# Performance work log

Measured on AMD Instinct MI355X. Metric: run time of the kernel, lower is better.

The kernel has to match this reference:

```python
import jax, jax.numpy as jnp
import numpy as np

H = 4          # number of GCN heads (hard-coded self.h = 4)
EPS = 1e-6     # MWPToolkit LayerNorm eps
B, K, D, HID = 16, 1024, 256, 256
DK = D // H


def setup_inputs() -> dict:
    key = jax.random.key(0)
    ks = jax.random.split(key, 12)
    sc = lambda fan_in: 1.0 / np.sqrt(fan_in).astype(np.float32)
    return {
        "graph_nodes": jax.random.normal(ks[0], (B, K, D), jnp.float32),
        "graph": jax.random.randint(ks[1], (B, 5, K, K), 0, 2, jnp.int32),
        # per-head GCN layer 1: GraphConvolution(indim -> hiddim)
        "Wg1": jax.random.normal(ks[2], (H, D, HID), jnp.float32) * sc(D),
        "bg1": jax.random.normal(ks[3], (H, HID), jnp.float32) * sc(D),
        # per-head GCN layer 2: GraphConvolution(hiddim -> d_k)
        "Wg2": jax.random.normal(ks[4], (H, HID, DK), jnp.float32) * sc(HID),
        "bg2": jax.random.normal(ks[5], (H, DK), jnp.float32) * sc(HID),
        # PositionwiseFeedForward: Linear(indim,hiddim) -> ReLU -> Linear(hiddim,outdim)
        "Wf1": jax.random.normal(ks[6], (D, HID), jnp.float32) * sc(D),
        "bf1": jax.random.normal(ks[7], (HID,), jnp.float32) * sc(D),
        "Wf2": jax.random.normal(ks[8], (HID, D), jnp.float32) * sc(HID),
        "bf2": jax.random.normal(ks[9], (D,), jnp.float32) * sc(HID),
        # LayerNorm(outdim) affine params
        "ln_a": jnp.ones((D,), jnp.float32),
        "ln_b": jnp.zeros((D,), jnp.float32),
    }


def reference(graph_nodes, graph, Wg1, bg1, Wg2, bg2, Wf1, bf1, Wf2, bf2, ln_a, ln_b):
    adj = graph.astype(jnp.float32)                      # (B, 5, K, K)
    # adj_list = [adj[:,1], adj[:,1], adj[:,4], adj[:,4]] -> stack heads
    adj_h = jnp.stack([adj[:, 1], adj[:, 1], adj[:, 4], adj[:, 4]])  # (H,B,K,K)

    # GCN layer 1 (all heads at once): relu(adj @ (x @ W1) + b1)
    sup1 = jnp.einsum('bkd,hdf->hbkf', graph_nodes, Wg1)            # (H,B,K,HID)
    h1 = jax.nn.relu(jnp.einsum('hbkj,hbjf->hbkf', adj_h, sup1)
                     + bg1[:, None, None, :])
    # (dropout is identity in eval)
    # GCN layer 2: adj @ (h1 @ W2) + b2
    sup2 = jnp.einsum('hbkf,hfe->hbke', h1, Wg2)                    # (H,B,K,DK)
    h2 = jnp.einsum('hbkj,hbje->hbke', adj_h, sup2) + bg2[:, None, None, :]

    # concat heads along feature dim: (B,K,H*DK) == (B,K,D)
    g = jnp.transpose(h2, (1, 2, 0, 3)).reshape(h2.shape[1], h2.shape[2], -1)

    # MWPToolkit LayerNorm: a*(x-mean)/(std+eps)+b, std unbiased (ddof=1)
    mu = g.mean(-1, keepdims=True)
    sd = jnp.std(g, axis=-1, keepdims=True, ddof=1)
    g = ln_a * (g - mu) / (sd + EPS) + ln_b + graph_nodes           # residual

    # PositionwiseFeedForward + residual (dropout identity in eval)
    ff = jax.nn.relu(g @ Wf1 + bf1) @ Wf2 + bf2
    out = ff + g
    return adj, out
```

## Files before the change

kernel.cpp:

```cpp
#include <hip/hip_runtime.h>

typedef unsigned short ushort_t;
using short8  = __attribute__((ext_vector_type(8))) short;
using floatx4 = __attribute__((ext_vector_type(4))) float;

__device__ __forceinline__ ushort_t f2bf(float f) {
  unsigned int x = __builtin_bit_cast(unsigned int, f);
  x += 0x7fffu + ((x >> 16) & 1u);
  return (ushort_t)(x >> 16);
}

__device__ __forceinline__ void gld16(const ushort_t* g, ushort_t* l) {
  __builtin_amdgcn_global_load_lds(
      (const __attribute__((address_space(1))) void*)(unsigned long long)(uintptr_t)g,
      (__attribute__((address_space(3))) void*)l, 16, 0, 0);
}

__global__ __launch_bounds__(256) void k_prep(const int* __restrict__ graph,
                                              float* __restrict__ adj_out,
                                              ushort_t* __restrict__ adjb,
                                              const float* __restrict__ gn,
                                              ushort_t* __restrict__ XT,
                                              const float* __restrict__ Wg1, const float* __restrict__ Wg2,
                                              const float* __restrict__ Wf1, const float* __restrict__ Wf2,
                                              ushort_t* __restrict__ W1T, ushort_t* __restrict__ W2pT,
                                              ushort_t* __restrict__ Wf1T, ushort_t* __restrict__ Wf2T) {
  __shared__ float t[64][68];
  const int bid = blockIdx.x;
  if (bid < 81920) {
    const size_t i = (size_t)bid * 256 + threadIdx.x;
    int4 v = ((const int4*)graph)[i];
    float4 f = make_float4((float)v.x, (float)v.y, (float)v.z, (float)v.w);
    ((float4*)adj_out)[i] = f;
    const size_t e0 = i * 4;
    const unsigned sb = (unsigned)(e0 >> 20);
    const unsigned s = sb % 5u, b = sb / 5u;
    if (s == 1u || s == 4u) {
      const unsigned tt = (s == 4u) ? 1u : 0u;
      ushort4 h;
      h.x = f2bf(f.x); h.y = f2bf(f.y); h.z = f2bf(f.z); h.w = f2bf(f.w);
      *(ushort4*)(adjb + (((size_t)(b * 2 + tt)) << 20) + (e0 & 0xFFFFFu)) = h;
    }
  } else if (bid < 82944) {
    const int id = bid - 81920;
    const int kt = id & 15, dt = (id >> 4) & 3, b = id >> 6;
    const int r  = threadIdx.x >> 4;
    const int c4 = (threadIdx.x & 15) * 4;
#pragma unroll
    for (int rr = 0; rr < 4; rr++) {
      const int kl = rr * 16 + r;
      float4 v = *(const float4*)(gn + ((size_t)(b * 1024 + kt * 64 + kl)) * 256 + dt * 64 + c4);
      t[kl][c4] = v.x; t[kl][c4 + 1] = v.y; t[kl][c4 + 2] = v.z; t[kl][c4 + 3] = v.w;
    }
    __syncthreads();
#pragma unroll
    for (int rr = 0; rr < 4; rr++) {
      const int dl = rr * 16 + r;
      ushort4 h;
      h.x = f2bf(t[c4][dl]);     h.y = f2bf(t[c4 + 1][dl]);
      h.z = f2bf(t[c4 + 2][dl]); h.w = f2bf(t[c4 + 3][dl]);
      *(ushort4*)(XT + ((size_t)(b * 256 + dt * 64 + dl)) * 1024 + kt * 64 + c4) = h;
    }
  } else {
    const int i = (bid - 82944) * 256 + threadIdx.x;
    if (i < 262144) {
      const int fI = i >> 8, d = i & 255;
      const int h = fI >> 8, ff = fI & 255;
      W1T[i] = f2bf(Wg1[((h << 8) + d) * 256 + ff]);
    } else if (i < 393216) {
      const int j = i - 262144;
      const int tt = j >> 16, rem = j & 65535;
      const int ep = rem >> 9, k = rem & 511;
      const int hh = ep >> 6;
      const float v = ((k >> 8) == hh)
          ? Wg2[(((tt * 2 + hh) << 8) + (k & 255)) * 64 + (ep & 63)] : 0.f;
      W2pT[j] = f2bf(v);
    } else if (i < 458752) {
      const int j = i - 393216;
      const int n = j >> 8, k = j & 255;
      Wf1T[j] = f2bf(Wf1[k * 256 + n]);
    } else if (i < 524288) {
      const int j = i - 458752;
      const int n = j >> 8, k = j & 255;
      Wf2T[j] = f2bf(Wf2[k * 256 + n]);
    }
  }
}

__global__ __launch_bounds__(256) void k_mid(const ushort_t* __restrict__ adjb,
                                             const ushort_t* __restrict__ XT,
                                             const ushort_t* __restrict__ W1T,
                                             const float* __restrict__ bg1,
                                             const ushort_t* __restrict__ W2pT,
                                             ushort_t* __restrict__ sup2T) {
  __shared__ ushort_t As[64 * 64];
  __shared__ ushort_t Bs[256 * 64];
  __shared__ ushort_t AXs[64 * 256];
  ushort_t* Hs = Bs + 8192;

  const int mt = blockIdx.x, bt = blockIdx.y;
  const int b = bt >> 1, t = bt & 1;
  const int tid = threadIdx.x, wave = tid >> 6, lane = tid & 63;
  const int l15 = lane & 15, quad = lane >> 4;
  const int wm = wave >> 1, wn = wave & 1;
  const int srow8 = lane >> 3, schunk = lane & 7;
  const int gcol = (schunk ^ srow8) * 8;
  const int cx = l15 & 7;

  const ushort_t* gA = adjb + ((size_t)bt << 20) + (size_t)(mt * 64 + wave * 16 + srow8) * 1024 + gcol;
  const ushort_t* gB = XT + ((size_t)b << 18) + (size_t)(wave * 64 + srow8) * 1024 + gcol;
  ushort_t* lA = As + (wave * 16) * 64;
  ushort_t* lB = Bs + (wave * 64) * 64;

  floatx4 acc1[2][8] = {};
  const int arow1 = (wm * 32 + l15) * 64;
  const int brow1 = (wn * 128 + l15) * 64;

  for (int k0 = 0; k0 < 1024; k0 += 64) {
#pragma unroll
    for (int ci = 0; ci < 2; ci++) gld16(gA + (size_t)(ci * 8) * 1024, lA + ci * 512);
#pragma unroll
    for (int ci = 0; ci < 8; ci++) gld16(gB + (size_t)(ci * 8) * 1024, lB + ci * 512);
    gA += 64; gB += 64;
    __syncthreads();
#pragma unroll
    for (int ks = 0; ks < 2; ks++) {
      const int cs = ((ks * 4 + quad) ^ cx) * 8;
      short8 af[2], bfr[8];
#pragma unroll
      for (int i = 0; i < 2; i++) af[i]  = *(const short8*)(As + arow1 + i * 1024 + cs);
#pragma unroll
      for (int j = 0; j < 8; j++) bfr[j] = *(const short8*)(Bs + brow1 + j * 1024 + cs);
#pragma unroll
      for (int i = 0; i < 2; i++)
#pragma unroll
        for (int j = 0; j < 8; j++)
          acc1[i][j] = __builtin_amdgcn_mfma_f32_16x16x32_bf16(af[i], bfr[j], acc1[i][j], 0, 0, 0);
    }
    __syncthreads();
  }

#pragma unroll
  for (int i = 0; i < 2; i++)
#pragma unroll
    for (int j = 0; j < 8; j++)
#pragma unroll
      for (int r = 0; r < 4; r++) {
        const int row = wm * 32 + i * 16 + quad * 4 + r;
        const int d   = wn * 128 + j * 16 + l15;
        AXs[row * 256 + ((((d >> 3) ^ row) & 31) << 3) + (d & 7)] = f2bf(acc1[i][j][r]);
      }
  __syncthreads();

  floatx4 acc4[4][2] = {};

#pragma unroll 1
  for (int nn = 0; nn < 4; nn++) {
    const int fg = t * 512 + nn * 128;

    floatx4 acc3[2][4] = {};
    for (int k0 = 0; k0 < 256; k0 += 64) {
#pragma unroll
      for (int ci = 0; ci < 4; ci++)
        gld16(W1T + (size_t)(fg + wave * 32 + ci * 8 + srow8) * 256 + k0 + gcol,
              Bs + (wave * 32 + ci * 8) * 64);
      __syncthreads();
#pragma unroll
      for (int ks = 0; ks < 2; ks++) {
        const int c32 = (k0 >> 3) + ks * 4 + quad;
        const int cs = ((ks * 4 + quad) ^ cx) * 8;
        short8 af[2], bfr[4];
#pragma unroll
        for (int i = 0; i < 2; i++) {
          const int row = wm * 32 + i * 16 + l15;
          af[i] = *(const short8*)(AXs + row * 256 + (((c32 ^ row) & 31) << 3));
        }
#pragma unroll
        for (int j = 0; j < 4; j++)
          bfr[j] = *(const short8*)(Bs + (wn * 64 + j * 16 + l15) * 64 + cs);
#pragma unroll
        for (int i = 0; i < 2; i++)
#pragma unroll
          for (int j = 0; j < 4; j++)
            acc3[i][j] = __builtin_amdgcn_mfma_f32_16x16x32_bf16(af[i], bfr[j], acc3[i][j], 0, 0, 0);
      }
      __syncthreads();
    }

#pragma unroll
    for (int j = 0; j < 4; j++) {
      const int fl = wn * 64 + j * 16 + l15;
      const float bj = bg1[fg + fl];
#pragma unroll
      for (int i = 0; i < 2; i++)
#pragma unroll
        for (int r = 0; r < 4; r++) {
          const int row = wm * 32 + i * 16 + quad * 4 + r;
          const float v = fmaxf(acc3[i][j][r] + bj, 0.f);
          Hs[row * 128 + ((((fl >> 3) ^ row) & 15) << 3) + (fl & 7)] = f2bf(v);
        }
    }
    __syncthreads();

    for (int k0 = 0; k0 < 128; k0 += 64) {
#pragma unroll
      for (int ci = 0; ci < 4; ci++)
        gld16(W2pT + (size_t)t * 65536 + (size_t)(wave * 32 + ci * 8 + srow8) * 512 + nn * 128 + k0 + gcol,
              Bs + (wave * 32 + ci * 8) * 64);
      __syncthreads();
#pragma unroll
      for (int ks = 0; ks < 2; ks++) {
        const int c32h = (k0 >> 3) + ks * 4 + quad;
        const int cs = ((ks * 4 + quad) ^ cx) * 8;
        short8 af[4], bfr[2];
#pragma unroll
        for (int i = 0; i < 4; i++)
          af[i] = *(const short8*)(Bs + (wm * 64 + i * 16 + l15) * 64 + cs);
#pragma unroll
        for (int j = 0; j < 2; j++) {
          const int row = wn * 32 + j * 16 + l15;
          bfr[j] = *(const short8*)(Hs + row * 128 + (((c32h ^ row) & 15) << 3));
        }
#pragma unroll
        for (int i = 0; i < 4; i++)
#pragma unroll
          for (int j = 0; j < 2; j++)
            acc4[i][j] = __builtin_amdgcn_mfma_f32_16x16x32_bf16(af[i], bfr[j], acc4[i][j], 0, 0, 0);
      }
      __syncthreads();
    }
  }

#pragma unroll
  for (int i = 0; i < 4; i++)
#pragma unroll
    for (int j = 0; j < 2; j++)
#pragma unroll
      for (int r = 0; r < 4; r++) {
        const int ep = wm * 64 + i * 16 + quad * 4 + r;
        const int kp = mt * 64 + wn * 32 + j * 16 + l15;
        sup2T[(size_t)bt * 131072 + (size_t)ep * 1024 + kp] = f2bf(acc4[i][j][r]);
      }
}

__global__ __launch_bounds__(256) void k_tail(const ushort_t* __restrict__ adjb,
                                              const ushort_t* __restrict__ sup2T,
                                              const float* __restrict__ bg2,
                                              const float* __restrict__ gn,
                                              const float* __restrict__ la,
                                              const float* __restrict__ lb,
                                              const ushort_t* __restrict__ Wf1T,
                                              const float* __restrict__ bf1,
                                              const ushort_t* __restrict__ Wf2T,
                                              const float* __restrict__ bf2,
                                              float* __restrict__ out) {
  __shared__ ushort_t As[64 * 64];
  __shared__ ushort_t Bs[256 * 64];
  __shared__ ushort_t Ps[32 * 256];
  __shared__ ushort_t Ts[32 * 256];
  __shared__ float sred[4][32], qred[4][32];

  const int mt = blockIdx.x, b = blockIdx.y;
  const int tid = threadIdx.x, wave = tid >> 6, lane = tid & 63;
  const int l15 = lane & 15, quad = lane >> 4;
  const int wn = wave;
  const int tsel = wn >> 1;

  const int srow8 = lane >> 3, schunk = lane & 7;
  const int gcol = (schunk ^ srow8) * 8;

  const ushort_t* gA = adjb + ((size_t)(b * 2 + (wave >> 1)) << 20)
                     + (size_t)(mt * 32 + (wave & 1) * 16 + srow8) * 1024 + gcol;
  const ushort_t* gB = sup2T + (size_t)(b * 2 + (wave >> 1)) * 131072
                     + (size_t)((wave & 1) * 64 + srow8) * 1024 + gcol;
  ushort_t* lA = As + (wave * 16) * 64;
  ushort_t* lB = Bs + (wave * 64) * 64;

  floatx4 acc[2][4] = {};
  const int arow0 = (tsel * 32 + l15) * 64;
  const int brow0 = (wn * 64 + l15) * 64;
  const int cx = l15 & 7;

  for (int k0 = 0; k0 < 1024; k0 += 64) {
#pragma unroll
    for (int ci = 0; ci < 2; ci++)
      gld16(gA + (size_t)(ci * 8) * 1024, lA + ci * 512);
#pragma unroll
    for (int ci = 0; ci < 8; ci++)
      gld16(gB + (size_t)(ci * 8) * 1024, lB + ci * 512);
    gA += 64; gB += 64;
    __syncthreads();
#pragma unroll
    for (int ks = 0; ks < 2; ks++) {
      const int cs = ((ks * 4 + quad) ^ cx) * 8;
      short8 af[2], bfr[4];
#pragma unroll
      for (int i = 0; i < 2; i++) af[i]  = *(const short8*)(As + arow0 + i * 1024 + cs);
#pragma unroll
      for (int j = 0; j < 4; j++) bfr[j] = *(const short8*)(Bs + brow0 + j * 1024 + cs);
#pragma unroll
      for (int i = 0; i < 2; i++)
#pragma unroll
        for (int j = 0; j < 4; j++)
          acc[i][j] = __builtin_amdgcn_mfma_f32_16x16x32_bf16(af[i], bfr[j], acc[i][j], 0, 0, 0);
    }
    __syncthreads();
  }

  float laj[4], lbj[4];
#pragma unroll
  for (int j = 0; j < 4; j++) {
    const int colg = wn * 64 + j * 16 + l15;
    const float bj = bg2[colg];
    laj[j] = la[colg]; lbj[j] = lb[colg];
#pragma unroll
    for (int i = 0; i < 2; i++)
#pragma unroll
      for (int r = 0; r < 4; r++) acc[i][j][r] += bj;
  }
#pragma unroll
  for (int i = 0; i < 2; i++)
#pragma unroll
    for (int r = 0; r < 4; r++) {
      float s = 0.f, q = 0.f;
#pragma unroll
      for (int j = 0; j < 4; j++) { const float v = acc[i][j][r]; s += v; q += v * v; }
#pragma unroll
      for (int m = 1; m < 16; m <<= 1) { s += __shfl_xor(s, m); q += __shfl_xor(q, m); }
      if (l15 == 0) {
        const int row = i * 16 + quad * 4 + r;
        sred[wn][row] = s; qred[wn][row] = q;
      }
    }
  __syncthreads();

  const size_t rowbase = (size_t)(b * 1024 + mt * 32);
  float glnreg[2][4][4];
#pragma unroll
  for (int i = 0; i < 2; i++)
#pragma unroll
    for (int r = 0; r < 4; r++) {
      const int row = i * 16 + quad * 4 + r;
      const float S = sred[0][row] + sred[1][row] + sred[2][row] + sred[3][row];
      const float Q = qred[0][row] + qred[1][row] + qred[2][row] + qred[3][row];
      const float mu = S * (1.f / 256.f);
      const float var = fmaxf((Q - S * mu) * (1.f / 255.f), 0.f);
      const float inv = 1.f / (sqrtf(var) + 1e-6f);
      const float* gnr = gn + (rowbase + row) * 256;
#pragma unroll
      for (int j = 0; j < 4; j++) {
        const int colg = wn * 64 + j * 16 + l15;
        const float g = laj[j] * (acc[i][j][r] - mu) * inv + lbj[j] + gnr[colg];
        glnreg[i][j][r] = g;
        Ps[row * 256 + ((((colg >> 3) ^ row) & 31) << 3) + (colg & 7)] = f2bf(g);
      }
    }
  __syncthreads();

  floatx4 acc2[2][4] = {};
  for (int k0 = 0; k0 < 256; k0 += 64) {
#pragma unroll
    for (int ci = 0; ci < 8; ci++)
      gld16(Wf1T + (size_t)(wave * 64 + ci * 8 + srow8) * 256 + k0 + gcol,
            Bs + (wave * 64 + ci * 8) * 64);
    __syncthreads();
#pragma unroll
    for (int ks = 0; ks < 2; ks++) {
      const int c32 = (k0 >> 3) + ks * 4 + quad;
      const int cs = ((ks * 4 + quad) ^ cx) * 8;
      short8 af[2], bfr[4];
#pragma unroll
      for (int i = 0; i < 2; i++) {
        const int row = i * 16 + l15;
        af[i] = *(const short8*)(Ps + row * 256 + (((c32 ^ row) & 31) << 3));
      }
#pragma unroll
      for (int j = 0; j < 4; j++) bfr[j] = *(const short8*)(Bs + brow0 + j * 1024 + cs);
#pragma unroll
      for (int i = 0; i < 2; i++)
#pragma unroll
        for (int j = 0; j < 4; j++)
          acc2[i][j] = __builtin_amdgcn_mfma_f32_16x16x32_bf16(af[i], bfr[j], acc2[i][j], 0, 0, 0);
    }
    __syncthreads();
  }

#pragma unroll
  for (int j = 0; j < 4; j++) {
    const int colg = wn * 64 + j * 16 + l15;
    const float bj = bf1[colg];
#pragma unroll
    for (int i = 0; i < 2; i++)
#pragma unroll
      for (int r = 0; r < 4; r++) {
        const int row = i * 16 + quad * 4 + r;
        const float v = fmaxf(acc2[i][j][r] + bj, 0.f);
        Ts[row * 256 + ((((colg >> 3) ^ row) & 31) << 3) + (colg & 7)] = f2bf(v);
      }
  }
  __syncthreads();

  floatx4 acc3[2][4] = {};
  for (int k0 = 0; k0 < 256; k0 += 64) {
#pragma unroll
    for (int ci = 0; ci < 8; ci++)
      gld16(Wf2T + (size_t)(wave * 64 + ci * 8 + srow8) * 256 + k0 + gcol,
            Bs + (wave * 64 + ci * 8) * 64);
    __syncthreads();
#pragma unroll
    for (int ks = 0; ks < 2; ks++) {
      const int c32 = (k0 >> 3) + ks * 4 + quad;
      const int cs = ((ks * 4 + quad) ^ cx) * 8;
      short8 af[2], bfr[4];
#pragma unroll
      for (int i = 0; i < 2; i++) {
        const int row = i * 16 + l15;
        af[i] = *(const short8*)(Ts + row * 256 + (((c32 ^ row) & 31) << 3));
      }
#pragma unroll
      for (int j = 0; j < 4; j++) bfr[j] = *(const short8*)(Bs + brow0 + j * 1024 + cs);
#pragma unroll
      for (int i = 0; i < 2; i++)
#pragma unroll
        for (int j = 0; j < 4; j++)
          acc3[i][j] = __builtin_amdgcn_mfma_f32_16x16x32_bf16(af[i], bfr[j], acc3[i][j], 0, 0, 0);
    }
    __syncthreads();
  }

#pragma unroll
  for (int j = 0; j < 4; j++) {
    const int colg = wn * 64 + j * 16 + l15;
    const float bj = bf2[colg];
#pragma unroll
    for (int i = 0; i < 2; i++)
#pragma unroll
      for (int r = 0; r < 4; r++) {
        const int row = i * 16 + quad * 4 + r;
        out[(rowbase + row) * 256 + colg] = acc3[i][j][r] + bj + glnreg[i][j][r];
      }
  }
}

extern "C" void kernel_launch(void* const* d_in, const int* in_sizes, int n_in,
                              void* d_out, int out_size, void* d_ws, size_t ws_size,
                              hipStream_t stream) {
  const float* gnodes = (const float*)d_in[0];
  const int*   graph  = (const int*)d_in[1];
  const float* Wg1 = (const float*)d_in[2];
  const float* bg1 = (const float*)d_in[3];
  const float* Wg2 = (const float*)d_in[4];
  const float* bg2 = (const float*)d_in[5];
  const float* Wf1 = (const float*)d_in[6];
  const float* bf1 = (const float*)d_in[7];
  const float* Wf2 = (const float*)d_in[8];
  const float* bf2 = (const float*)d_in[9];
  const float* ln_a = (const float*)d_in[10];
  const float* ln_b = (const float*)d_in[11];

  float* adj_out = (float*)d_out;
  float* out     = (float*)d_out + 83886080;

  char* ws = (char*)d_ws;
  ushort_t* adjb  = (ushort_t*)(ws);
  ushort_t* XT    = (ushort_t*)(ws + 67108864);
  ushort_t* W1T   = (ushort_t*)(ws + 75497472);
  ushort_t* W2pT  = (ushort_t*)(ws + 76021760);
  ushort_t* Wf1T  = (ushort_t*)(ws + 76283904);
  ushort_t* Wf2T  = (ushort_t*)(ws + 76414976);
  ushort_t* sup2T = (ushort_t*)(ws + 76546048);

  k_prep<<<84992, 256, 0, stream>>>(graph, adj_out, adjb, gnodes, XT,
                                    Wg1, Wg2, Wf1, Wf2, W1T, W2pT, Wf1T, Wf2T);

  k_mid<<<dim3(16, 32), 256, 0, stream>>>(adjb, XT, W1T, bg1, W2pT, sup2T);

  k_tail<<<dim3(32, 16), 256, 0, stream>>>(adjb, sup2T, bg2, gnodes, ln_a, ln_b,
                                           Wf1T, bf1, Wf2T, bf2, out);
}
```

Measured before the change: 656.5 us.

## Double-buffer GEMM main loops and prefetch weight tiles in GCN kernels

Rewrites the adjacency-GEMM K loops in k_mid and k_tail as two-stage ping-pong pipelines. The next tile's global-to-LDS loads are issued before the current tile's MFMAs, with a single waitcnt+barrier per stage replacing the paired __syncthreads. Weight tiles for the follow-on GEMMs (W1, W2, Wf1, Wf2) are also prefetched ahead of the epilogues. It further adds launch_bounds min-2-blocks occupancy hints and nontemporal loads/stores for the large adjacency conversion and the output. The aim is to hide global memory latency behind MFMA work. The cost is more LDS aliasing, and the FFN loops refill a shared weight buffer without a block barrier, which risks cross-wave races.

```diff
diff --git a/kernel.cpp b/kernel.cpp
--- a/kernel.cpp
+++ b/kernel.cpp
@@ -3,6 +3,8 @@
 typedef unsigned short ushort_t;
 using short8  = __attribute__((ext_vector_type(8))) short;
 using floatx4 = __attribute__((ext_vector_type(4))) float;
+using intx4   = __attribute__((ext_vector_type(4))) int;
+using fx4     = __attribute__((ext_vector_type(4))) float;
 
 __device__ __forceinline__ ushort_t f2bf(float f) {
   unsigned int x = __builtin_bit_cast(unsigned int, f);
@@ -14,6 +16,20 @@
   __builtin_amdgcn_global_load_lds(
       (const __attribute__((address_space(1))) void*)(unsigned long long)(uintptr_t)g,
       (__attribute__((address_space(3))) void*)l, 16, 0, 0);
+}
+
+__device__ __forceinline__ void wait_bar() {
+  asm volatile("s_waitcnt vmcnt(0)" ::: "memory");
+  __builtin_amdgcn_s_barrier();
+  __builtin_amdgcn_sched_barrier(0);
+}
+__device__ __forceinline__ void vwait0() {
+  asm volatile("s_waitcnt vmcnt(0)" ::: "memory");
+  __builtin_amdgcn_sched_barrier(0);
+}
+__device__ __forceinline__ void lwait0() {
+  asm volatile("s_waitcnt lgkmcnt(0)" ::: "memory");
+  __builtin_amdgcn_sched_barrier(0);
 }
 
 __global__ __launch_bounds__(256) void k_prep(const int* __restrict__ graph,
@@ -29,16 +45,16 @@
   const int bid = blockIdx.x;
   if (bid < 81920) {
     const size_t i = (size_t)bid * 256 + threadIdx.x;
-    int4 v = ((const int4*)graph)[i];
-    float4 f = make_float4((float)v.x, (float)v.y, (float)v.z, (float)v.w);
-    ((float4*)adj_out)[i] = f;
+    intx4 v = __builtin_nontemporal_load((const intx4*)graph + i);
+    fx4 f; f[0] = (float)v[0]; f[1] = (float)v[1]; f[2] = (float)v[2]; f[3] = (float)v[3];
+    __builtin_nontemporal_store(f, (fx4*)adj_out + i);
     const size_t e0 = i * 4;
     const unsigned sb = (unsigned)(e0 >> 20);
     const unsigned s = sb % 5u, b = sb / 5u;
     if (s == 1u || s == 4u) {
       const unsigned tt = (s == 4u) ? 1u : 0u;
       ushort4 h;
-      h.x = f2bf(f.x); h.y = f2bf(f.y); h.z = f2bf(f.z); h.w = f2bf(f.w);
+      h.x = f2bf(f[0]); h.y = f2bf(f[1]); h.z = f2bf(f[2]); h.w = f2bf(f[3]);
       *(ushort4*)(adjb + (((size_t)(b * 2 + tt)) << 20) + (e0 & 0xFFFFFu)) = h;
     }
   } else if (bid < 82944) {
@@ -87,16 +103,17 @@
   }
 }
 
-__global__ __launch_bounds__(256) void k_mid(const ushort_t* __restrict__ adjb,
-                                             const ushort_t* __restrict__ XT,
-                                             const ushort_t* __restrict__ W1T,
-                                             const float* __restrict__ bg1,
-                                             const ushort_t* __restrict__ W2pT,
-                                             ushort_t* __restrict__ sup2T) {
-  __shared__ ushort_t As[64 * 64];
-  __shared__ ushort_t Bs[256 * 64];
-  __shared__ ushort_t AXs[64 * 256];
+__global__ __launch_bounds__(256, 2) void k_mid(const ushort_t* __restrict__ adjb,
+                                                const ushort_t* __restrict__ XT,
+                                                const ushort_t* __restrict__ W1T,
+                                                const float* __restrict__ bg1,
+                                                const ushort_t* __restrict__ W2pT,
+                                                ushort_t* __restrict__ sup2T) {
+  __shared__ __align__(16) ushort_t As[2][4096];
+  __shared__ __align__(16) ushort_t Bs[16384];
+  __shared__ __align__(16) ushort_t AXs[16384];
   ushort_t* Hs = Bs + 8192;
+  ushort_t* Asf = &As[0][0];
 
   const int mt = blockIdx.x, bt = blockIdx.y;
   const int b = bt >> 1, t = bt & 1;
@@ -109,36 +126,50 @@
 
   const ushort_t* gA = adjb + ((size_t)bt << 20) + (size_t)(mt * 64 + wave * 16 + srow8) * 1024 + gcol;
   const ushort_t* gB = XT + ((size_t)b << 18) + (size_t)(wave * 64 + srow8) * 1024 + gcol;
-  ushort_t* lA = As + (wave * 16) * 64;
-  ushort_t* lB = Bs + (wave * 64) * 64;
+  ushort_t* lA0 = &As[0][0] + wave * 1024;
+  ushort_t* lA1 = &As[1][0] + wave * 1024;
+  ushort_t* lB0 = Bs + wave * 4096;
+  ushort_t* lB1 = AXs + wave * 4096;
 
   floatx4 acc1[2][8] = {};
   const int arow1 = (wm * 32 + l15) * 64;
   const int brow1 = (wn * 128 + l15) * 64;
 
-  for (int k0 = 0; k0 < 1024; k0 += 64) {
-#pragma unroll
-    for (int ci = 0; ci < 2; ci++) gld16(gA + (size_t)(ci * 8) * 1024, lA + ci * 512);
-#pragma unroll
-    for (int ci = 0; ci < 8; ci++) gld16(gB + (size_t)(ci * 8) * 1024, lB + ci * 512);
-    gA += 64; gB += 64;
-    __syncthreads();
-#pragma unroll
-    for (int ks = 0; ks < 2; ks++) {
-      const int cs = ((ks * 4 + quad) ^ cx) * 8;
-      short8 af[2], bfr[8];
-#pragma unroll
-      for (int i = 0; i < 2; i++) af[i]  = *(const short8*)(As + arow1 + i * 1024 + cs);
-#pragma unroll
-      for (int j = 0; j < 8; j++) bfr[j] = *(const short8*)(Bs + brow1 + j * 1024 + cs);
-#pragma unroll
-      for (int i = 0; i < 2; i++)
-#pragma unroll
-        for (int j = 0; j < 8; j++)
-          acc1[i][j] = __builtin_amdgcn_mfma_f32_16x16x32_bf16(af[i], bfr[j], acc1[i][j], 0, 0, 0);
-    }
-    __syncthreads();
-  }
+#define STAGE1(LA, LB, KOFF) do { \
+  _Pragma("unroll") for (int ci = 0; ci < 2; ci++) gld16(gA + (size_t)(KOFF) + (size_t)(ci * 8) * 1024, (LA) + ci * 512); \
+  _Pragma("unroll") for (int ci = 0; ci < 8; ci++) gld16(gB + (size_t)(KOFF) + (size_t)(ci * 8) * 1024, (LB) + ci * 512); \
+} while (0)
+
+#define MM1(AB, BB) do { \
+  _Pragma("unroll") for (int ks = 0; ks < 2; ks++) { \
+    const int cs = ((ks * 4 + quad) ^ cx) * 8; \
+    short8 af[2], bfr[8]; \
+    _Pragma("unroll") for (int i = 0; i < 2; i++) af[i]  = *(const short8*)((AB) + arow1 + i * 1024 + cs); \
+    _Pragma("unroll") for (int j = 0; j < 8; j++) bfr[j] = *(const short8*)((BB) + brow1 + j * 1024 + cs); \
+    _Pragma("unroll") for (int i = 0; i < 2; i++) \
+      _Pragma("unroll") for (int j = 0; j < 8; j++) \
+        acc1[i][j] = __builtin_amdgcn_mfma_f32_16x16x32_bf16(af[i], bfr[j], acc1[i][j], 0, 0, 0); \
+  } \
+} while (0)
+
+  STAGE1(lA0, lB0, 0);
+  wait_bar();
+#pragma unroll 1
+  for (int k0 = 0; k0 < 1024; k0 += 128) {
+    STAGE1(lA1, lB1, k0 + 64);
+    MM1(&As[0][0], Bs);
+    wait_bar();
+    if (k0 + 128 < 1024) STAGE1(lA0, lB0, k0 + 128);
+    MM1(&As[1][0], AXs);
+    wait_bar();
+  }
+
+#define STAGE3(DST, FG, KOFF) do { \
+  _Pragma("unroll") for (int ci = 0; ci < 4; ci++) \
+    gld16(W1T + (size_t)((FG) + wave * 32 + ci * 8 + srow8) * 256 + (KOFF) + gcol, (DST) + (wave * 32 + ci * 8) * 64); \
+} while (0)
+
+  STAGE3(Bs, t * 512, 0);
 
 #pragma unroll
   for (int i = 0; i < 2; i++)
@@ -154,38 +185,56 @@
 
   floatx4 acc4[4][2] = {};
 
+#define MM3(BB, K0) do { \
+  _Pragma("unroll") for (int ks = 0; ks < 2; ks++) { \
+    const int c32 = ((K0) >> 3) + ks * 4 + quad; \
+    const int cs = ((ks * 4 + quad) ^ cx) * 8; \
+    short8 af[2], bfr[4]; \
+    _Pragma("unroll") for (int i = 0; i < 2; i++) { \
+      const int row = wm * 32 + i * 16 + l15; \
+      af[i] = *(const short8*)(AXs + row * 256 + (((c32 ^ row) & 31) << 3)); \
+    } \
+    _Pragma("unroll") for (int j = 0; j < 4; j++) \
+      bfr[j] = *(const short8*)((BB) + (wn * 64 + j * 16 + l15) * 64 + cs); \
+    _Pragma("unroll") for (int i = 0; i < 2; i++) \
+      _Pragma("unroll") for (int j = 0; j < 4; j++) \
+        acc3[i][j] = __builtin_amdgcn_mfma_f32_16x16x32_bf16(af[i], bfr[j], acc3[i][j], 0, 0, 0); \
+  } \
+} while (0)
+
+#define STAGE4(DST, KOFF) do { \
+  _Pragma("unroll") for (int ci = 0; ci < 4; ci++) \
+    gld16(W2pT + (size_t)t * 65536 + (size_t)(wave * 32 + ci * 8 + srow8) * 512 + nn * 128 + (KOFF) + gcol, \
+          (DST) + (wave * 32 + ci * 8) * 64); \
+} while (0)
+
+#define MM4(BB, K0) do { \
+  _Pragma("unroll") for (int ks = 0; ks < 2; ks++) { \
+    const int c32h = ((K0) >> 3) + ks * 4 + quad; \
+    const int cs = ((ks * 4 + quad) ^ cx) * 8; \
+    short8 af[4], bfr[2]; \
+    _Pragma("unroll") for (int i = 0; i < 4; i++) \
+      af[i] = *(const short8*)((BB) + (wm * 64 + i * 16 + l15) * 64 + cs); \
+    _Pragma("unroll") for (int j = 0; j < 2; j++) { \
+      const int row = wn * 32 + j * 16 + l15; \
+      bfr[j] = *(const short8*)(Hs + row * 128 + (((c32h ^ row) & 15) << 3)); \
+    } \
+    _Pragma("unroll") for (int i = 0; i < 4; i++) \
+      _Pragma("unroll") for (int j = 0; j < 2; j++) \
+        acc4[i][j] = __builtin_amdgcn_mfma_f32_16x16x32_bf16(af[i], bfr[j], acc4[i][j], 0, 0, 0); \
+  } \
+} while (0)
+
 #pragma unroll 1
   for (int nn = 0; nn < 4; nn++) {
     const int fg = t * 512 + nn * 128;
-
     floatx4 acc3[2][4] = {};
-    for (int k0 = 0; k0 < 256; k0 += 64) {
-#pragma unroll
-      for (int ci = 0; ci < 4; ci++)
-        gld16(W1T + (size_t)(fg + wave * 32 + ci * 8 + srow8) * 256 + k0 + gcol,
-              Bs + (wave * 32 + ci * 8) * 64);
-      __syncthreads();
-#pragma unroll
-      for (int ks = 0; ks < 2; ks++) {
-        const int c32 = (k0 >> 3) + ks * 4 + quad;
-        const int cs = ((ks * 4 + quad) ^ cx) * 8;
-        short8 af[2], bfr[4];
-#pragma unroll
-        for (int i = 0; i < 2; i++) {
-          const int row = wm * 32 + i * 16 + l15;
-          af[i] = *(const short8*)(AXs + row * 256 + (((c32 ^ row) & 31) << 3));
-        }
-#pragma unroll
-        for (int j = 0; j < 4; j++)
-          bfr[j] = *(const short8*)(Bs + (wn * 64 + j * 16 + l15) * 64 + cs);
-#pragma unroll
-        for (int i = 0; i < 2; i++)
-#pragma unroll
-          for (int j = 0; j < 4; j++)
-            acc3[i][j] = __builtin_amdgcn_mfma_f32_16x16x32_bf16(af[i], bfr[j], acc3[i][j], 0, 0, 0);
-      }
-      __syncthreads();
-    }
+
+    STAGE3(Asf, fg, 64);  MM3(Bs, 0);    wait_bar();
+    STAGE3(Bs, fg, 128);  MM3(Asf, 64);  wait_bar();
+    STAGE3(Asf, fg, 192); MM3(Bs, 128);  wait_bar();
+    MM3(Asf, 192);
+    STAGE4(Bs, 0);
 
 #pragma unroll
     for (int j = 0; j < 4; j++) {
@@ -202,33 +251,10 @@
     }
     __syncthreads();
 
-    for (int k0 = 0; k0 < 128; k0 += 64) {
-#pragma unroll
-      for (int ci = 0; ci < 4; ci++)
-        gld16(W2pT + (size_t)t * 65536 + (size_t)(wave * 32 + ci * 8 + srow8) * 512 + nn * 128 + k0 + gcol,
-              Bs + (wave * 32 + ci * 8) * 64);
-      __syncthreads();
-#pragma unroll
-      for (int ks = 0; ks < 2; ks++) {
-        const int c32h = (k0 >> 3) + ks * 4 + quad;
-        const int cs = ((ks * 4 + quad) ^ cx) * 8;
-        short8 af[4], bfr[2];
-#pragma unroll
-        for (int i = 0; i < 4; i++)
-          af[i] = *(const short8*)(Bs + (wm * 64 + i * 16 + l15) * 64 + cs);
-#pragma unroll
-        for (int j = 0; j < 2; j++) {
-          const int row = wn * 32 + j * 16 + l15;
-          bfr[j] = *(const short8*)(Hs + row * 128 + (((c32h ^ row) & 15) << 3));
-        }
-#pragma unroll
-        for (int i = 0; i < 4; i++)
-#pragma unroll
-          for (int j = 0; j < 2; j++)
-            acc4[i][j] = __builtin_amdgcn_mfma_f32_16x16x32_bf16(af[i], bfr[j], acc4[i][j], 0, 0, 0);
-      }
-      __syncthreads();
-    }
+    STAGE4(Asf, 64);  MM4(Bs, 0);  wait_bar();
+    MM4(Asf, 64);
+    if (nn < 3) STAGE3(Bs, t * 512 + (nn + 1) * 128, 0);
+    wait_bar();
   }
 
 #pragma unroll
@@ -241,24 +267,34 @@
         const int kp = mt * 64 + wn * 32 + j * 16 + l15;
         sup2T[(size_t)bt * 131072 + (size_t)ep * 1024 + kp] = f2bf(acc4[i][j][r]);
       }
-}
-
-__global__ __launch_bounds__(256) void k_tail(const ushort_t* __restrict__ adjb,
-                                              const ushort_t* __restrict__ sup2T,
-                                              const float* __restrict__ bg2,
-                                              const float* __restrict__ gn,
-                                              const float* __restrict__ la,
-                                              const float* __restrict__ lb,
-                                              const ushort_t* __restrict__ Wf1T,
-                                              const float* __restrict__ bf1,
-                                              const ushort_t* __restrict__ Wf2T,
-                                              const float* __restrict__ bf2,
-                                              float* __restrict__ out) {
-  __shared__ ushort_t As[64 * 64];
-  __shared__ ushort_t Bs[256 * 64];
-  __shared__ ushort_t Ps[32 * 256];
-  __shared__ ushort_t Ts[32 * 256];
-  __shared__ float sred[4][32], qred[4][32];
+#undef STAGE1
+#undef MM1
+#undef STAGE3
+#undef MM3
+#undef STAGE4
+#undef MM4
+}
+
+__global__ __launch_bounds__(256, 2) void k_tail(const ushort_t* __restrict__ adjb,
+                                                 const ushort_t* __restrict__ sup2T,
+                                                 const float* __restrict__ bg2,
+                                                 const float* __restrict__ gn,
+                                                 const float* __restrict__ la,
+                                                 const float* __restrict__ lb,
+                                                 const ushort_t* __restrict__ Wf1T,
+                                                 const float* __restrict__ bf1,
+                                                 const ushort_t* __restrict__ Wf2T,
+                                                 const float* __restrict__ bf2,
+                                                 float* __restrict__ out) {
+  __shared__ __align__(16) ushort_t SH[40960];
+  ushort_t* A0  = SH;
+  ushort_t* A1  = SH + 4096;
+  ushort_t* BsT = SH + 8192;
+  ushort_t* PT  = SH + 24576;
+  ushort_t* Ps  = PT;
+  ushort_t* Ts  = PT + 8192;
+  float* sred = (float*)SH;
+  float* qred = (float*)SH + 128;
 
   const int mt = blockIdx.x, b = blockIdx.y;
   const int tid = threadIdx.x, wave = tid >> 6, lane = tid & 63;
@@ -273,39 +309,51 @@
                      + (size_t)(mt * 32 + (wave & 1) * 16 + srow8) * 1024 + gcol;
   const ushort_t* gB = sup2T + (size_t)(b * 2 + (wave >> 1)) * 131072
                      + (size_t)((wave & 1) * 64 + srow8) * 1024 + gcol;
-  ushort_t* lA = As + (wave * 16) * 64;
-  ushort_t* lB = Bs + (wave * 64) * 64;
+  ushort_t* lA0 = A0 + wave * 1024;
+  ushort_t* lA1 = A1 + wave * 1024;
+  ushort_t* lB0 = BsT + wave * 4096;
+  ushort_t* lB1 = PT + wave * 4096;
 
   floatx4 acc[2][4] = {};
   const int arow0 = (tsel * 32 + l15) * 64;
   const int brow0 = (wn * 64 + l15) * 64;
   const int cx = l15 & 7;
 
-  for (int k0 = 0; k0 < 1024; k0 += 64) {
-#pragma unroll
-    for (int ci = 0; ci < 2; ci++)
-      gld16(gA + (size_t)(ci * 8) * 1024, lA + ci * 512);
-#pragma unroll
-    for (int ci = 0; ci < 8; ci++)
-      gld16(gB + (size_t)(ci * 8) * 1024, lB + ci * 512);
-    gA += 64; gB += 64;
-    __syncthreads();
-#pragma unroll
-    for (int ks = 0; ks < 2; ks++) {
-      const int cs = ((ks * 4 + quad) ^ cx) * 8;
-      short8 af[2], bfr[4];
-#pragma unroll
-      for (int i = 0; i < 2; i++) af[i]  = *(const short8*)(As + arow0 + i * 1024 + cs);
-#pragma unroll
-      for (int j = 0; j < 4; j++) bfr[j] = *(const short8*)(Bs + brow0 + j * 1024 + cs);
-#pragma unroll
-      for (int i = 0; i < 2; i++)
-#pragma unroll
-        for (int j = 0; j < 4; j++)
-          acc[i][j] = __builtin_amdgcn_mfma_f32_16x16x32_bf16(af[i], bfr[j], acc[i][j], 0, 0, 0);
-    }
-    __syncthreads();
-  }
+#define TSTAGE1(LA, LB, KOFF) do { \
+  _Pragma("unroll") for (int ci = 0; ci < 2; ci++) gld16(gA + (size_t)(KOFF) + (size_t)(ci * 8) * 1024, (LA) + ci * 512); \
+  _Pragma("unroll") for (int ci = 0; ci < 8; ci++) gld16(gB + (size_t)(KOFF) + (size_t)(ci * 8) * 1024, (LB) + ci * 512); \
+} while (0)
+
+#define TMM1(AB, BB) do { \
+  _Pragma("unroll") for (int ks = 0; ks < 2; ks++) { \
+    const int cs = ((ks * 4 + quad) ^ cx) * 8; \
+    short8 af[2], bfr[4]; \
+    _Pragma("unroll") for (int i = 0; i < 2; i++) af[i]  = *(const short8*)((AB) + arow0 + i * 1024 + cs); \
+    _Pragma("unroll") for (int j = 0; j < 4; j++) bfr[j] = *(const short8*)((BB) + brow0 + j * 1024 + cs); \
+    _Pragma("unroll") for (int i = 0; i < 2; i++) \
+      _Pragma("unroll") for (int j = 0; j < 4; j++) \
+        acc[i][j] = __builtin_amdgcn_mfma_f32_16x16x32_bf16(af[i], bfr[j], acc[i][j], 0, 0, 0); \
+  } \
+} while (0)
+
+  TSTAGE1(lA0, lB0, 0);
+  wait_bar();
+#pragma unroll 1
+  for (int k0 = 0; k0 < 1024; k0 += 128) {
+    TSTAGE1(lA1, lB1, k0 + 64);
+    TMM1(A0, BsT);
+    wait_bar();
+    if (k0 + 128 < 1024) TSTAGE1(lA0, lB0, k0 + 128);
+    TMM1(A1, PT);
+    wait_bar();
+  }
+
+#define TSTAGEF(W, DST, KOFF) do { \
+  _Pragma("unroll") for (int ci = 0; ci < 8; ci++) \
+    gld16((W) + (size_t)(wave * 64 + ci * 8 + srow8) * 256 + (KOFF) + gcol, (DST) + (wave * 64 + ci * 8) * 64); \
+} while (0)
+
+  TSTAGEF(Wf1T, BsT, 0);
 
   float laj[4], lbj[4];
 #pragma unroll
@@ -329,7 +377,7 @@
       for (int m = 1; m < 16; m <<= 1) { s += __shfl_xor(s, m); q += __shfl_xor(q, m); }
       if (l15 == 0) {
         const int row = i * 16 + quad * 4 + r;
-        sred[wn][row] = s; qred[wn][row] = q;
+        sred[wn * 32 + row] = s; qred[wn * 32 + row] = q;
       }
     }
   __syncthreads();
@@ -341,8 +389,8 @@
 #pragma unroll
     for (int r = 0; r < 4; r++) {
       const int row = i * 16 + quad * 4 + r;
-      const float S = sred[0][row] + sred[1][row] + sred[2][row] + sred[3][row];
-      const float Q = qred[0][row] + qred[1][row] + qred[2][row] + qred[3][row];
+      const float S = sred[row] + sred[32 + row] + sred[64 + row] + sred[96 + row];
+      const float Q = qred[row] + qred[32 + row] + qred[64 + row] + qred[96 + row];
       const float mu = S * (1.f / 256.f);
       const float var = fmaxf((Q - S * mu) * (1.f / 255.f), 0.f);
       const float inv = 1.f / (sqrtf(var) + 1e-6f);
@@ -358,32 +406,35 @@
   __syncthreads();
 
   floatx4 acc2[2][4] = {};
+#pragma unroll 1
   for (int k0 = 0; k0 < 256; k0 += 64) {
-#pragma unroll
-    for (int ci = 0; ci < 8; ci++)
-      gld16(Wf1T + (size_t)(wave * 64 + ci * 8 + srow8) * 256 + k0 + gcol,
-            Bs + (wave * 64 + ci * 8) * 64);
-    __syncthreads();
+    vwait0();
+    short8 af[2][2], bfr[2][4];
 #pragma unroll
     for (int ks = 0; ks < 2; ks++) {
       const int c32 = (k0 >> 3) + ks * 4 + quad;
       const int cs = ((ks * 4 + quad) ^ cx) * 8;
-      short8 af[2], bfr[4];
 #pragma unroll
       for (int i = 0; i < 2; i++) {
         const int row = i * 16 + l15;
-        af[i] = *(const short8*)(Ps + row * 256 + (((c32 ^ row) & 31) << 3));
-      }
-#pragma unroll
-      for (int j = 0; j < 4; j++) bfr[j] = *(const short8*)(Bs + brow0 + j * 1024 + cs);
+        af[ks][i] = *(const short8*)(Ps + row * 256 + (((c32 ^ row) & 31) << 3));
+      }
+#pragma unroll
+      for (int j = 0; j < 4; j++)
+        bfr[ks][j] = *(const short8*)(BsT + brow0 + j * 1024 + cs);
+    }
+    lwait0();
+    if (k0 < 192) TSTAGEF(Wf1T, BsT, k0 + 64);
+#pragma unroll
+    for (int ks = 0; ks < 2; ks++)
 #pragma unroll
       for (int i = 0; i < 2; i++)
 #pragma unroll
         for (int j = 0; j < 4; j++)
-          acc2[i][j] = __builtin_amdgcn_mfma_f32_16x16x32_bf16(af[i], bfr[j], acc2[i][j], 0, 0, 0);
-    }
-    __syncthreads();
-  }
+          acc2[i][j] = __builtin_amdgcn_mfma_f32_16x16x32_bf16(af[ks][i], bfr[ks][j], acc2[i][j], 0, 0, 0);
+  }
+
+  TSTAGEF(Wf2T, BsT, 0);
 
 #pragma unroll
   for (int j = 0; j < 4; j++) {
@@ -400,32 +451,33 @@
   }
   __syncthreads();
 
-  floatx4 acc3[2][4] = {};
+  floatx4 acc3f[2][4] = {};
+#pragma unroll 1
   for (int k0 = 0; k0 < 256; k0 += 64) {
-#pragma unroll
-    for (int ci = 0; ci < 8; ci++)
-      gld16(Wf2T + (size_t)(wave * 64 + ci * 8 + srow8) * 256 + k0 + gcol,
-            Bs + (wave * 64 + ci * 8) * 64);
-    __syncthreads();
+    vwait0();
+    short8 af[2][2], bfr[2][4];
 #pragma unroll
     for (int ks = 0; ks < 2; ks++) {
       const int c32 = (k0 >> 3) + ks * 4 + quad;
       const int cs = ((ks * 4 + quad) ^ cx) * 8;
-      short8 af[2], bfr[4];
 #pragma unroll
       for (int i = 0; i < 2; i++) {
         const int row = i * 16 + l15;
-        af[i] = *(const short8*)(Ts + row * 256 + (((c32 ^ row) & 31) << 3));
-      }
-#pragma unroll
-      for (int j = 0; j < 4; j++) bfr[j] = *(const short8*)(Bs + brow0 + j * 1024 + cs);
+        af[ks][i] = *(const short8*)(Ts + row * 256 + (((c32 ^ row) & 31) << 3));
+      }
+#pragma unroll
+      for (int j = 0; j < 4; j++)
+        bfr[ks][j] = *(const short8*)(BsT + brow0 + j * 1024 + cs);
+    }
+    lwait0();
+    if (k0 < 192) TSTAGEF(Wf2T, BsT, k0 + 64);
+#pragma unroll
+    for (int ks = 0; ks < 2; ks++)
 #pragma unroll
       for (int i = 0; i < 2; i++)
 #pragma unroll
         for (int j = 0; j < 4; j++)
-          acc3[i][j] = __builtin_amdgcn_mfma_f32_16x16x32_bf16(af[i], bfr[j], acc3[i][j], 0, 0, 0);
-    }
-    __syncthreads();
+          acc3f[i][j] = __builtin_amdgcn_mfma_f32_16x16x32_bf16(af[ks][i], bfr[ks][j], acc3f[i][j], 0, 0, 0);
   }
 
 #pragma unroll
@@ -437,9 +489,13 @@
 #pragma unroll
       for (int r = 0; r < 4; r++) {
         const int row = i * 16 + quad * 4 + r;
-        out[(rowbase + row) * 256 + colg] = acc3[i][j][r] + bj + glnreg[i][j][r];
-      }
-  }
+        __builtin_nontemporal_store(acc3f[i][j][r] + bj + glnreg[i][j][r],
+                                    &out[(rowbase + row) * 256 + colg]);
+      }
+  }
+#undef TSTAGE1
+#undef TMM1
+#undef TSTAGEF
 }
 
 extern "C" void kernel_launch(void* const* d_in, const int* in_sizes, int n_in,
```

Measured after the change: 638.5 us. 2.7% less time.
